# Optimization experiments

Hardware: AMD Instinct MI355X
Metric: run time of the kernel (lower is better)

The kernel has to match this reference:

```python
import jax, jax.numpy as jnp
import numpy as np

MASK_FILL = -1e10
LOG_2PI = float(np.log(2.0 * np.pi))


def setup_inputs() -> dict:
    key = jax.random.key(0)
    k1, k2, k3 = jax.random.split(key, 3)
    bs, seq_len, emb_dim = 32, 512, 512
    T = 2048
    emb = jax.random.normal(k1, (bs, seq_len, emb_dim), dtype=jnp.float32)
    # positive durations; rescale so the max total duration over the batch == T exactly,
    # matching torch's T = sum(durations).int().max()
    d = jax.random.uniform(k2, (bs, seq_len), dtype=jnp.float32, minval=0.5, maxval=1.0)
    d = d * (T / jnp.max(jnp.sum(d, axis=1)))
    log_sigma = jax.random.normal(k3, (1,), dtype=jnp.float32) * 0.1
    return {"emb": emb, "durations": d, "log_sigma": log_sigma, "T": T}


def reference(emb, durations, log_sigma, T):
    # emb: (bs, S, E); durations: (bs, S); log_sigma: (1,); T: static int
    bs, S, E = emb.shape
    ls = log_sigma[0]
    sigma = jnp.exp(ls)
    # Gaussian centers per token: cumsum - 0.5*dur  -> (bs, S)
    centers = jnp.cumsum(durations, axis=1) - 0.5 * durations
    t = jnp.arange(T, dtype=emb.dtype)  # frame indices (T,)
    # Normal(loc=centers, scale=sigma).log_prob(t + 0.5)  -> (bs, T, S)
    z = (t[None, :, None] + 0.5 - centers[:, None, :]) / sigma
    logp = -0.5 * z * z - ls - 0.5 * LOG_2PI
    # mask out zero-duration tokens
    logp = jnp.where((durations == 0.0)[:, None, :], MASK_FILL, logp)
    w = jax.nn.softmax(logp, axis=2)  # (bs, T, S)
    x = jnp.einsum('bts,bse->bte', w, emb)  # (bs, T, E)
    total = jnp.sum(durations, axis=1)  # (bs,)
    out_mask = t[None, :] < total[:, None]  # (bs, T) bool
    return x, out_mask
```

## Files before the change

kernel.cpp:

```cpp
#include <hip/hip_runtime.h>
#include <math.h>

#define BS 32
#define S_TOK 512
#define E_DIM 512
#define T_FR 2048
#define FPB 8
#define WMAX 20
#define THRESH -25.0f



typedef float vfloat4 __attribute__((ext_vector_type(4)));

__global__ __launch_bounds__(256, 8) void fused_all(
    const float* __restrict__ emb,
    const float* __restrict__ dur,
    const float* __restrict__ log_sigma,
    float* __restrict__ x,
    float* __restrict__ mask_out) {
  int id = blockIdx.x;
  int sw = ((id & 7) << 10) + (id >> 3);
  int b = sw >> 8;
  int t0 = (sw & 255) << 3;

  int tid = threadIdx.x;
  int grp = tid >> 7;
  int col = tid & 127;

  __shared__ float cbS[S_TOK];
  __shared__ __align__(16) float wT[WMAX][FPB];
  __shared__ float mS[FPB];
  __shared__ float invS[FPB];
  __shared__ double wsumS[4];
  __shared__ int histS[FPB];
  __shared__ int n0S[4];
  __shared__ int uloS, cntS;
  __shared__ float totalS;

  if (tid < FPB) histS[tid] = 0;

  float inv_sigma = expf(-log_sigma[0]);
  float tq0 = (float)t0 + 0.5f;
  float tq7 = (float)t0 + 7.5f;

  {
    const float* dp = dur + b * S_TOK;
    int i2 = tid << 1;
    double d0 = (double)dp[i2];
    double d1 = (double)dp[i2 + 1];
    double pair = d0 + d1;
    double run = pair;
#pragma unroll
    for (int off = 1; off < 64; off <<= 1) {
      double v = __shfl_up(run, off, 64);
      if ((tid & 63) >= off) run += v;
    }
    int w = tid >> 6;
    if ((tid & 63) == 63) wsumS[w] = run;
    __syncthreads();
    double wexcl = 0.0;
#pragma unroll
    for (int k = 0; k < 3; ++k) wexcl += (k < w) ? wsumS[k] : 0.0;
    double incl = wexcl + run;
    double excl = incl - pair;
    float c0 = (float)(excl + d0 - 0.5 * d0);
    float c1 = (float)(excl + (d0 + d1) - 0.5 * d1);
    cbS[i2] = c0;
    cbS[i2 + 1] = c1;

    int n0 = (c0 < tq0 ? 1 : 0) + (c1 < tq0 ? 1 : 0);
    if (c0 >= tq0 && c0 < tq7) atomicAdd(&histS[(int)floorf(c0 - tq0) + 1], 1);
    if (c1 >= tq0 && c1 < tq7) atomicAdd(&histS[(int)floorf(c1 - tq0) + 1], 1);
#pragma unroll
    for (int off = 1; off < 64; off <<= 1) n0 += __shfl_xor(n0, off, 64);
    if ((tid & 63) == 0) n0S[w] = n0;
    if (tid == 255) totalS = (float)incl;
  }
  __syncthreads();

  if (tid < 64) {
    int l = tid;
    int sc = (l >= 1 && l < FPB) ? histS[l] : 0;
#pragma unroll
    for (int off = 1; off < FPB; off <<= 1) {
      int v = __shfl_up(sc, off, 64);
      if (l >= off) sc += v;
    }
    int N0 = n0S[0] + n0S[1] + n0S[2] + n0S[3];
    int best = 0;
    float m = 0.0f;
    if (l < FPB) {
      int N = N0 + sc;
      float tqf = (float)(t0 + l) + 0.5f;
      if (N <= 0) {
        best = 0;
        float z = (tqf - cbS[0]) * inv_sigma; m = -0.5f * z * z;
      } else if (N >= S_TOK) {
        best = S_TOK - 1;
        float z = (tqf - cbS[best]) * inv_sigma; m = -0.5f * z * z;
      } else {
        float za = (tqf - cbS[N - 1]) * inv_sigma; float va = -0.5f * za * za;
        float zb = (tqf - cbS[N]) * inv_sigma;     float vb = -0.5f * zb * zb;
        if (va >= vb) { best = N - 1; m = va; } else { best = N; m = vb; }
      }
      mS[l] = m;
    }
    int best0 = __shfl(best, 0, 64);  float m0 = __shfl(m, 0, 64);
    int best7 = __shfl(best, 7, 64);  float m7 = __shfl(m, 7, 64);
    int p = l & 15;
    bool flag = false;
    if (l < 16) {
      int s = best0 - 1 - p;
      if (s >= 0) {
        float z = (tq0 - cbS[s]) * inv_sigma;
        flag = (-0.5f * z * z) > m0 + THRESH;
      }
    } else if (l < 32) {
      int s = best7 + 1 + p;
      if (s < S_TOK) {
        float z = (tq7 - cbS[s]) * inv_sigma;
        flag = (-0.5f * z * z) > m7 + THRESH;
      }
    }
    unsigned long long bal = __ballot(flag);
    if (l == 0) {
      int wl = best0 - __popcll(bal & 0xFFFFull);
      int wh = best7 + __popcll(bal & 0xFFFF0000ull);
      uloS = wl;
      cntS = min(wh - wl + 1, WMAX);
    }
  }
  __syncthreads();

  int ulo = uloS, cnt = cntS;

  const vfloat4* e4 =
      (const vfloat4*)emb + ((size_t)(b * S_TOK + ulo)) * (E_DIM / 4) + col;
  vfloat4 vcur = e4[0];
  vfloat4 vnext = e4[(size_t)min(1, cnt - 1) * (E_DIM / 4)];

  if (tid < cnt * FPB) {
    int i = tid >> 3, f = tid & 7;
    float c = cbS[ulo + i];
    float tqf = (float)(t0 + f) + 0.5f;
    float z = (tqf - c) * inv_sigma;
    float v = -0.5f * z * z;
    wT[i][f] = expf(v - mS[f]);
  }
  __syncthreads();

  {
    int f = tid >> 5, p = tid & 31;
    float s = 0.0f;
    for (int i = p; i < cnt; i += 32) s += wT[i][f];
#pragma unroll
    for (int off = 1; off < 32; off <<= 1) s += __shfl_xor(s, off, 64);
    if (p == 0) invS[f] = 1.0f / s;
  }
  __syncthreads();

  vfloat4 acc0 = {0.f,0.f,0.f,0.f}, acc1 = {0.f,0.f,0.f,0.f};
  vfloat4 acc2 = {0.f,0.f,0.f,0.f}, acc3 = {0.f,0.f,0.f,0.f};

  for (int i = 0; i < cnt; ++i) {
    vfloat4 vfut = e4[(size_t)min(i + 2, cnt - 1) * (E_DIM / 4)];
    vfloat4 w = *(const vfloat4*)&wT[i][grp << 2];
    acc0 += w.x * vcur;
    acc1 += w.y * vcur;
    acc2 += w.z * vcur;
    acc3 += w.w * vcur;
    vcur = vnext; vnext = vfut;
  }

  int f0 = grp << 2;
  vfloat4* xp = (vfloat4*)x +
      ((size_t)(b * T_FR + t0 + f0)) * (E_DIM / 4) + col;
  xp[0 * (E_DIM / 4)] = acc0 * invS[f0 + 0];
  xp[1 * (E_DIM / 4)] = acc1 * invS[f0 + 1];
  xp[2 * (E_DIM / 4)] = acc2 * invS[f0 + 2];
  xp[3 * (E_DIM / 4)] = acc3 * invS[f0 + 3];

  if (tid < FPB) {
    int t = t0 + tid;
    mask_out[b * T_FR + t] = ((float)t < totalS) ? 1.0f : 0.0f;
  }
}

extern "C" void kernel_launch(void* const* d_in, const int* in_sizes, int n_in,
                              void* d_out, int out_size, void* d_ws,
                              size_t ws_size, hipStream_t stream) {
  const float* emb = (const float*)d_in[0];
  const float* dur = (const float*)d_in[1];
  const float* log_sigma = (const float*)d_in[2];

  float* x = (float*)d_out;
  float* mask_out = x + (size_t)BS * T_FR * E_DIM;

  fused_all<<<(BS * T_FR) / FPB, 256, 0, stream>>>(
      emb, dur, log_sigma, x, mask_out);
}
```

Baseline: 166.3 us.

## Process four frame tiles per block to amortize duration cumsum

Each block now loops over four 8-frame tiles of the same batch row. The double-precision duration scan and center computation run once per block instead of once per tile, and the grid shrinks by a factor of four with a new batch-to-XCD mapping. The per-tile histogram/atomic search for the nearest center is replaced by a binary search over the shared centers. The trade-off is fewer resident blocks and serialized tiles with extra barriers, which may reduce latency hiding.

New measurement: 171.0 us. 2.8% more time.

```diff
diff --git a/kernel.cpp b/kernel.cpp
--- a/kernel.cpp
+++ b/kernel.cpp
@@ -6,6 +6,7 @@
 #define E_DIM 512
 #define T_FR 2048
 #define FPB 8
+#define NTILE 4
 #define WMAX 20
 #define THRESH -25.0f
 
@@ -20,9 +21,11 @@
     float* __restrict__ x,
     float* __restrict__ mask_out) {
   int id = blockIdx.x;
-  int sw = ((id & 7) << 10) + (id >> 3);
-  int b = sw >> 8;
-  int t0 = (sw & 255) << 3;
+  int xcd = id & 7;
+  int j = id >> 3;
+  int b = (xcd << 2) + (j >> 6);
+  int base = j & 63;
+  int rs = id & 3;
 
   int tid = threadIdx.x;
   int grp = tid >> 7;
@@ -33,16 +36,10 @@
   __shared__ float mS[FPB];
   __shared__ float invS[FPB];
   __shared__ double wsumS[4];
-  __shared__ int histS[FPB];
-  __shared__ int n0S[4];
   __shared__ int uloS, cntS;
   __shared__ float totalS;
 
-  if (tid < FPB) histS[tid] = 0;
-
   float inv_sigma = expf(-log_sigma[0]);
-  float tq0 = (float)t0 + 0.5f;
-  float tq7 = (float)t0 + 7.5f;
 
   {
     const float* dp = dur + b * S_TOK;
@@ -64,126 +61,119 @@
     for (int k = 0; k < 3; ++k) wexcl += (k < w) ? wsumS[k] : 0.0;
     double incl = wexcl + run;
     double excl = incl - pair;
-    float c0 = (float)(excl + d0 - 0.5 * d0);
-    float c1 = (float)(excl + (d0 + d1) - 0.5 * d1);
-    cbS[i2] = c0;
-    cbS[i2 + 1] = c1;
-
-    int n0 = (c0 < tq0 ? 1 : 0) + (c1 < tq0 ? 1 : 0);
-    if (c0 >= tq0 && c0 < tq7) atomicAdd(&histS[(int)floorf(c0 - tq0) + 1], 1);
-    if (c1 >= tq0 && c1 < tq7) atomicAdd(&histS[(int)floorf(c1 - tq0) + 1], 1);
-#pragma unroll
-    for (int off = 1; off < 64; off <<= 1) n0 += __shfl_xor(n0, off, 64);
-    if ((tid & 63) == 0) n0S[w] = n0;
+    cbS[i2]     = (float)(excl + d0 - 0.5 * d0);
+    cbS[i2 + 1] = (float)(excl + (d0 + d1) - 0.5 * d1);
     if (tid == 255) totalS = (float)incl;
   }
   __syncthreads();
 
-  if (tid < 64) {
-    int l = tid;
-    int sc = (l >= 1 && l < FPB) ? histS[l] : 0;
-#pragma unroll
-    for (int off = 1; off < FPB; off <<= 1) {
-      int v = __shfl_up(sc, off, 64);
-      if (l >= off) sc += v;
-    }
-    int N0 = n0S[0] + n0S[1] + n0S[2] + n0S[3];
-    int best = 0;
-    float m = 0.0f;
-    if (l < FPB) {
-      int N = N0 + sc;
-      float tqf = (float)(t0 + l) + 0.5f;
-      if (N <= 0) {
-        best = 0;
-        float z = (tqf - cbS[0]) * inv_sigma; m = -0.5f * z * z;
-      } else if (N >= S_TOK) {
-        best = S_TOK - 1;
-        float z = (tqf - cbS[best]) * inv_sigma; m = -0.5f * z * z;
-      } else {
-        float za = (tqf - cbS[N - 1]) * inv_sigma; float va = -0.5f * za * za;
-        float zb = (tqf - cbS[N]) * inv_sigma;     float vb = -0.5f * zb * zb;
-        if (va >= vb) { best = N - 1; m = va; } else { best = N; m = vb; }
+  for (int k = 0; k < NTILE; ++k) {
+    int t0 = (base + (((rs + k) & 3) << 6)) << 3;
+
+    if (tid < 64) {
+      int l = tid;
+      float tq0 = (float)t0 + 0.5f;
+      float tq7 = (float)t0 + 7.5f;
+      int best = 0;
+      float m = 0.0f;
+      if (l < FPB) {
+        float tqf = (float)(t0 + l) + 0.5f;
+        int lo = 0, hi = S_TOK;
+        while (lo < hi) {
+          int mid = (lo + hi) >> 1;
+          if (cbS[mid] < tqf) lo = mid + 1; else hi = mid;
+        }
+        if (lo == 0) {
+          best = 0;
+          float z = (tqf - cbS[0]) * inv_sigma; m = -0.5f * z * z;
+        } else if (lo == S_TOK) {
+          best = S_TOK - 1;
+          float z = (tqf - cbS[best]) * inv_sigma; m = -0.5f * z * z;
+        } else {
+          float za = (tqf - cbS[lo - 1]) * inv_sigma; float va = -0.5f * za * za;
+          float zb = (tqf - cbS[lo]) * inv_sigma;     float vb = -0.5f * zb * zb;
+          if (va >= vb) { best = lo - 1; m = va; } else { best = lo; m = vb; }
+        }
+        mS[l] = m;
       }
-      mS[l] = m;
-    }
-    int best0 = __shfl(best, 0, 64);  float m0 = __shfl(m, 0, 64);
-    int best7 = __shfl(best, 7, 64);  float m7 = __shfl(m, 7, 64);
-    int p = l & 15;
-    bool flag = false;
-    if (l < 16) {
-      int s = best0 - 1 - p;
-      if (s >= 0) {
-        float z = (tq0 - cbS[s]) * inv_sigma;
-        flag = (-0.5f * z * z) > m0 + THRESH;
+      int best0 = __shfl(best, 0, 64);  float m0 = __shfl(m, 0, 64);
+      int best7 = __shfl(best, 7, 64);  float m7 = __shfl(m, 7, 64);
+      int p = l & 15;
+      bool flag = false;
+      if (l < 16) {
+        int s = best0 - 1 - p;
+        if (s >= 0) {
+          float z = (tq0 - cbS[s]) * inv_sigma;
+          flag = (-0.5f * z * z) > m0 + THRESH;
+        }
+      } else if (l < 32) {
+        int s = best7 + 1 + p;
+        if (s < S_TOK) {
+          float z = (tq7 - cbS[s]) * inv_sigma;
+          flag = (-0.5f * z * z) > m7 + THRESH;
+        }
       }
-    } else if (l < 32) {
-      int s = best7 + 1 + p;
-      if (s < S_TOK) {
-        float z = (tq7 - cbS[s]) * inv_sigma;
-        flag = (-0.5f * z * z) > m7 + THRESH;
+      unsigned long long bal = __ballot(flag);
+      if (l == 0) {
+        int wl = best0 - __popcll(bal & 0xFFFFull);
+        int wh = best7 + __popcll(bal & 0xFFFF0000ull);
+        uloS = wl;
+        cntS = min(wh - wl + 1, WMAX);
       }
     }
-    unsigned long long bal = __ballot(flag);
-    if (l == 0) {
-      int wl = best0 - __popcll(bal & 0xFFFFull);
-      int wh = best7 + __popcll(bal & 0xFFFF0000ull);
-      uloS = wl;
-      cntS = min(wh - wl + 1, WMAX);
+    __syncthreads();
+
+    int ulo = uloS, cnt = cntS;
+
+    const vfloat4* e4 =
+        (const vfloat4*)emb + ((size_t)(b * S_TOK + ulo)) * (E_DIM / 4) + col;
+    vfloat4 vcur = e4[0];
+    vfloat4 vnext = e4[(size_t)min(1, cnt - 1) * (E_DIM / 4)];
+
+    if (tid < cnt * FPB) {
+      int i = tid >> 3, f = tid & 7;
+      float c = cbS[ulo + i];
+      float tqf = (float)(t0 + f) + 0.5f;
+      float z = (tqf - c) * inv_sigma;
+      wT[i][f] = expf(-0.5f * z * z - mS[f]);
     }
-  }
-  __syncthreads();
+    __syncthreads();
 
-  int ulo = uloS, cnt = cntS;
+    {
+      int f = tid >> 5, p = tid & 31;
+      float s = 0.0f;
+      for (int i = p; i < cnt; i += 32) s += wT[i][f];
+#pragma unroll
+      for (int off = 1; off < 32; off <<= 1) s += __shfl_xor(s, off, 64);
+      if (p == 0) invS[f] = 1.0f / s;
+    }
+    __syncthreads();
 
-  const vfloat4* e4 =
-      (const vfloat4*)emb + ((size_t)(b * S_TOK + ulo)) * (E_DIM / 4) + col;
-  vfloat4 vcur = e4[0];
-  vfloat4 vnext = e4[(size_t)min(1, cnt - 1) * (E_DIM / 4)];
+    vfloat4 acc0 = {0.f,0.f,0.f,0.f}, acc1 = {0.f,0.f,0.f,0.f};
+    vfloat4 acc2 = {0.f,0.f,0.f,0.f}, acc3 = {0.f,0.f,0.f,0.f};
 
-  if (tid < cnt * FPB) {
-    int i = tid >> 3, f = tid & 7;
-    float c = cbS[ulo + i];
-    float tqf = (float)(t0 + f) + 0.5f;
-    float z = (tqf - c) * inv_sigma;
-    float v = -0.5f * z * z;
-    wT[i][f] = expf(v - mS[f]);
-  }
-  __syncthreads();
+    for (int i = 0; i < cnt; ++i) {
+      vfloat4 vfut = e4[(size_t)min(i + 2, cnt - 1) * (E_DIM / 4)];
+      vfloat4 w = *(const vfloat4*)&wT[i][grp << 2];
+      acc0 += w.x * vcur;
+      acc1 += w.y * vcur;
+      acc2 += w.z * vcur;
+      acc3 += w.w * vcur;
+      vcur = vnext; vnext = vfut;
+    }
 
-  {
-    int f = tid >> 5, p = tid & 31;
-    float s = 0.0f;
-    for (int i = p; i < cnt; i += 32) s += wT[i][f];
-#pragma unroll
-    for (int off = 1; off < 32; off <<= 1) s += __shfl_xor(s, off, 64);
-    if (p == 0) invS[f] = 1.0f / s;
-  }
-  __syncthreads();
+    int f0 = grp << 2;
+    vfloat4* xp = (vfloat4*)x +
+        ((size_t)(b * T_FR + t0 + f0)) * (E_DIM / 4) + col;
+    xp[0 * (E_DIM / 4)] = acc0 * invS[f0 + 0];
+    xp[1 * (E_DIM / 4)] = acc1 * invS[f0 + 1];
+    xp[2 * (E_DIM / 4)] = acc2 * invS[f0 + 2];
+    xp[3 * (E_DIM / 4)] = acc3 * invS[f0 + 3];
 
-  vfloat4 acc0 = {0.f,0.f,0.f,0.f}, acc1 = {0.f,0.f,0.f,0.f};
-  vfloat4 acc2 = {0.f,0.f,0.f,0.f}, acc3 = {0.f,0.f,0.f,0.f};
-
-  for (int i = 0; i < cnt; ++i) {
-    vfloat4 vfut = e4[(size_t)min(i + 2, cnt - 1) * (E_DIM / 4)];
-    vfloat4 w = *(const vfloat4*)&wT[i][grp << 2];
-    acc0 += w.x * vcur;
-    acc1 += w.y * vcur;
-    acc2 += w.z * vcur;
-    acc3 += w.w * vcur;
-    vcur = vnext; vnext = vfut;
-  }
-
-  int f0 = grp << 2;
-  vfloat4* xp = (vfloat4*)x +
-      ((size_t)(b * T_FR + t0 + f0)) * (E_DIM / 4) + col;
-  xp[0 * (E_DIM / 4)] = acc0 * invS[f0 + 0];
-  xp[1 * (E_DIM / 4)] = acc1 * invS[f0 + 1];
-  xp[2 * (E_DIM / 4)] = acc2 * invS[f0 + 2];
-  xp[3 * (E_DIM / 4)] = acc3 * invS[f0 + 3];
-
-  if (tid < FPB) {
-    int t = t0 + tid;
-    mask_out[b * T_FR + t] = ((float)t < totalS) ? 1.0f : 0.0f;
+    if (tid < FPB) {
+      int t = t0 + tid;
+      mask_out[b * T_FR + t] = ((float)t < totalS) ? 1.0f : 0.0f;
+    }
   }
 }
 
@@ -197,6 +187,6 @@
   float* x = (float*)d_out;
   float* mask_out = x + (size_t)BS * T_FR * E_DIM;
 
-  fused_all<<<(BS * T_FR) / FPB, 256, 0, stream>>>(
+  fused_all<<<(BS * T_FR) / (FPB * NTILE), 256, 0, stream>>>(
       emb, dur, log_sigma, x, mask_out);
 }
```
